# Optimization experiments

Hardware: AMD Instinct MI355X
Metric: run time of the kernel (lower is better)

Reference implementation:

```python
import jax, jax.numpy as jnp
import numpy as np
from jax import lax


def setup_inputs() -> dict:
    key = jax.random.key(0)
    W = 32
    x = jax.random.normal(key, (32, 8192, 128), dtype=jnp.float32)
    weights = jnp.arange(1, W + 1, dtype=jnp.float32)  # [1, 2, ..., W]
    return {"x": x, "weights": weights, "window_size": W}


def reference(x, weights, window_size):
    # x: [B, T, C]; weights: [W] = [1..W]
    B, T, C = x.shape
    W = window_size
    # Zero-pad the front: with kernel [1..W], a VALID causal conv applies weight
    # (W - i + j) to x[j] within the window ending at i, which matches the
    # original's weights[-L:] slicing for partial windows (L = i + 1 < W).
    xp = jnp.pad(x, ((0, 0), (W - 1, 0), (0, 0)))  # [B, T+W-1, C]
    # Depthwise conv: same kernel per channel, feature_group_count = C.
    kernel = jnp.broadcast_to(weights[:, None, None], (W, 1, C))  # WIO
    numer = lax.conv_general_dilated(
        xp, kernel, window_strides=(1,), padding="VALID",
        dimension_numbers=("NWC", "WIO", "NWC"), feature_group_count=C,
    )  # [B, T, C]
    # denom[i] = sum of the last min(i+1, W) weights = cumsum(weights[::-1]) clipped.
    csum_rev = jnp.cumsum(weights[::-1])  # [W]
    idx = jnp.minimum(jnp.arange(T), W - 1)
    denom = csum_rev[idx]  # [T]
    return numer / denom[None, :, None]
```

## Files before the change

### kernel.cpp

```cpp
#include <hip/hip_runtime.h>


constexpr int W    = 32;
constexpr int B    = 32;
constexpr int T    = 8192;
constexpr int C    = 128;
constexpr int SEG  = 128;
constexpr int NSEG = T / SEG;

__global__ __launch_bounds__(256)
void wma_kernel(const float* __restrict__ x, float* __restrict__ out) {
    int gtid = blockIdx.x * blockDim.x + threadIdx.x;
    int c    = gtid % C;
    int rest = gtid / C;
    int seg  = rest % NSEG;
    int b    = rest / NSEG;
    if (b >= B) return;

    const int t0 = seg * SEG;
    const float* px = x   + ((size_t)b * T + t0) * C + c;
    float*       po = out + ((size_t)b * T + t0) * C + c;

    float hist[W];
    float S = 0.0f, N = 0.0f;
    int startChunk = 0;

    if (t0 == 0) {
        #pragma unroll
        for (int i = 0; i < W; ++i) hist[i] = 0.0f;
        #pragma unroll
        for (int i = 0; i < W; ++i) {
            float xn = px[i * C];
            N = N - S + 32.0f * xn;
            S = S - hist[i] + xn;
            hist[i] = xn;
            constexpr int full = 528;
            const float invd = 1.0f / (float)(full - (31 - i) * (32 - i) / 2);
            po[i * C] = N * invd;
        }
        startChunk = 1;
    } else {
        #pragma unroll
        for (int i = 0; i < W; ++i) hist[i] = px[(i - W) * C];
        #pragma unroll
        for (int i = 0; i < W; ++i) {
            S += hist[i];
            N += (float)(i + 1) * hist[i];
        }
    }

    const float invD = 1.0f / 528.0f;
    for (int ch = startChunk; ch < SEG / W; ++ch) {
        const float* pxc = px + (size_t)ch * W * C;
        float*       poc = po + (size_t)ch * W * C;
        #pragma unroll
        for (int i = 0; i < W; ++i) {
            float xn = pxc[i * C];
            N = N - S + 32.0f * xn;
            S = S - hist[i] + xn;
            hist[i] = xn;
            poc[i * C] = N * invD;
        }
    }
}

extern "C" void kernel_launch(void* const* d_in, const int* in_sizes, int n_in,
                              void* d_out, int out_size, void* d_ws, size_t ws_size,
                              hipStream_t stream) {
    const float* x = (const float*)d_in[0];
    float* out = (float*)d_out;

    const int total_threads = B * C * NSEG;
    dim3 grid(total_threads / 256), block(256);
    hipLaunchKernelGGL(wma_kernel, grid, block, 0, stream, x, out);
}
```

Measured before the change: 49.21 us.

## Vectorize channels into float4 per thread and use nontemporal stores

Each thread now processes four adjacent channels with 128-bit loads and stores, cutting the thread count by four. Output writes use nontemporal stores to avoid polluting caches. The grid shrinks to far fewer blocks, which risks leaving many compute units idle. The per-thread history register footprint also grows fourfold.

```diff
diff --git a/kernel.cpp b/kernel.cpp
--- a/kernel.cpp
+++ b/kernel.cpp
@@ -1,47 +1,49 @@
 #include <hip/hip_runtime.h>
 
+
+typedef float f32x4 __attribute__((ext_vector_type(4)));
 
 constexpr int W    = 32;
 constexpr int B    = 32;
 constexpr int T    = 8192;
 constexpr int C    = 128;
+constexpr int CQ   = C / 4;
 constexpr int SEG  = 128;
 constexpr int NSEG = T / SEG;
 
-__global__ __launch_bounds__(256)
+__global__ __launch_bounds__(256, 1)
 void wma_kernel(const float* __restrict__ x, float* __restrict__ out) {
     int gtid = blockIdx.x * blockDim.x + threadIdx.x;
-    int c    = gtid % C;
-    int rest = gtid / C;
+    int p    = gtid % CQ;
+    int rest = gtid / CQ;
     int seg  = rest % NSEG;
     int b    = rest / NSEG;
-    if (b >= B) return;
 
     const int t0 = seg * SEG;
-    const float* px = x   + ((size_t)b * T + t0) * C + c;
-    float*       po = out + ((size_t)b * T + t0) * C + c;
+    const f32x4* px = (const f32x4*)(x   + ((size_t)b * T + t0) * C) + p;
+    f32x4*       po = (f32x4*)      (out + ((size_t)b * T + t0) * C) + p;
 
-    float hist[W];
-    float S = 0.0f, N = 0.0f;
+    f32x4 hist[W];
+    f32x4 S = (f32x4)(0.f), N = (f32x4)(0.f);
     int startChunk = 0;
 
     if (t0 == 0) {
         #pragma unroll
-        for (int i = 0; i < W; ++i) hist[i] = 0.0f;
+        for (int i = 0; i < W; ++i) hist[i] = (f32x4)(0.f);
         #pragma unroll
         for (int i = 0; i < W; ++i) {
-            float xn = px[i * C];
+            f32x4 xn = px[i * CQ];
             N = N - S + 32.0f * xn;
             S = S - hist[i] + xn;
             hist[i] = xn;
-            constexpr int full = 528;
-            const float invd = 1.0f / (float)(full - (31 - i) * (32 - i) / 2);
-            po[i * C] = N * invd;
+            const float invd = 1.0f / (float)(528 - (31 - i) * (32 - i) / 2);
+            f32x4 o = N * invd;
+            __builtin_nontemporal_store(o, &po[i * CQ]);
         }
         startChunk = 1;
     } else {
         #pragma unroll
-        for (int i = 0; i < W; ++i) hist[i] = px[(i - W) * C];
+        for (int i = 0; i < W; ++i) hist[i] = px[(i - W) * CQ];
         #pragma unroll
         for (int i = 0; i < W; ++i) {
             S += hist[i];
@@ -51,15 +53,16 @@
 
     const float invD = 1.0f / 528.0f;
     for (int ch = startChunk; ch < SEG / W; ++ch) {
-        const float* pxc = px + (size_t)ch * W * C;
-        float*       poc = po + (size_t)ch * W * C;
+        const f32x4* pxc = px + (size_t)ch * W * CQ;
+        f32x4*       poc = po + (size_t)ch * W * CQ;
         #pragma unroll
         for (int i = 0; i < W; ++i) {
-            float xn = pxc[i * C];
+            f32x4 xn = pxc[i * CQ];
             N = N - S + 32.0f * xn;
             S = S - hist[i] + xn;
             hist[i] = xn;
-            poc[i * C] = N * invD;
+            f32x4 o = N * invD;
+            __builtin_nontemporal_store(o, &poc[i * CQ]);
         }
     }
 }
@@ -70,7 +73,7 @@
     const float* x = (const float*)d_in[0];
     float* out = (float*)d_out;
 
-    const int total_threads = B * C * NSEG;
+    const int total_threads = B * CQ * NSEG;
     dim3 grid(total_threads / 256), block(256);
     hipLaunchKernelGGL(wma_kernel, grid, block, 0, stream, x, out);
 }
```

Result: no change. 49.86 us (+1.3%).
